# Kernel optimization log

Hardware: AMD Instinct MI355X
Metric: run time of the kernel (lower is better)

The kernel has to match this reference:

```python
import jax, jax.numpy as jnp
import numpy as np

TEMPERATURE = 0.5
NUM_NEG_CANDIDATES = 8
HARD_NEG_K = 3


def setup_inputs() -> dict:
    key = jax.random.key(0)
    k1, k2 = jax.random.split(key)
    features = jax.random.normal(k1, (8192, 512), dtype=jnp.float32)
    labels = jax.random.randint(k2, (8192,), 0, 64, dtype=jnp.int64)
    return {"features": features, "labels": labels}


def reference(features, labels):
    B = features.shape[0]
    labels = labels.reshape(-1)
    # L2-normalize rows (torch F.normalize, eps=1e-12)
    f = features / jnp.maximum(jnp.linalg.norm(features, axis=1, keepdims=True), 1e-12)

    same = labels[:, None] == labels[None, :]          # [B, B]
    eye = jnp.eye(B, dtype=bool)
    neg_inf = jnp.float32(-jnp.inf)

    # Deterministic replacement for torch's randint/randperm sampling:
    # Gumbel-max = uniform sampling of one positive; Gumbel-top-m = sampling
    # m negatives without replacement.
    kp, kn = jax.random.split(jax.random.key(42))
    g_pos = jax.random.gumbel(kp, (B, B), dtype=jnp.float32)
    g_neg = jax.random.gumbel(kn, (B, B), dtype=jnp.float32)

    pos_mask = same & ~eye
    pos_j = jnp.argmax(jnp.where(pos_mask, g_pos, neg_inf), axis=1)   # [B]

    _, neg_idx = jax.lax.top_k(jnp.where(~same, g_neg, neg_inf), NUM_NEG_CANDIDATES)  # [B, m]

    cand = f[neg_idx]                                  # [B, m, D]
    neg_sims = jnp.einsum('bd,bmd->bm', f, cand)       # [B, m]
    hard_sims, _ = jax.lax.top_k(neg_sims, HARD_NEG_K)  # [B, k] hardest negatives

    pos_logit = jnp.sum(f * f[pos_j], axis=1) / TEMPERATURE          # [B]
    logits = jnp.concatenate([pos_logit[:, None], hard_sims / TEMPERATURE], axis=1)  # [B, 1+k]
    # cross-entropy with target index 0
    loss = jax.nn.logsumexp(logits, axis=1) - logits[:, 0]
    return jnp.mean(loss)
```

## Files before the change

### kernel.cpp

```cpp
#include <hip/hip_runtime.h>
#include <hip/hip_bf16.h>
#include <stdint.h>

#define BB 8192
#define DD 512
#define NNEG 8
#define CAP 256

#define VTHI 4273471488u

__host__ __device__ __forceinline__ uint32_t rotl32(uint32_t x, int r) {
#if defined(__HIP_DEVICE_COMPILE__)
  return __builtin_amdgcn_alignbit(x, x, 32 - r);
#else
  return (x << r) | (x >> (32 - r));
#endif
}

#define TF_RND(x0, x1, R) { x0 += x1; x1 = rotl32(x1, R); x1 ^= x0; }

__host__ __device__ __forceinline__ void threefry2x32(uint32_t k0, uint32_t k1,
                                                      uint32_t x0, uint32_t x1,
                                                      uint32_t& o0, uint32_t& o1) {
  uint32_t ks2 = k0 ^ k1 ^ 0x1BD11BDAu;
  x0 += k0; x1 += k1;
  TF_RND(x0, x1, 13) TF_RND(x0, x1, 15) TF_RND(x0, x1, 26) TF_RND(x0, x1, 6)
  x0 += k1; x1 += ks2 + 1u;
  TF_RND(x0, x1, 17) TF_RND(x0, x1, 29) TF_RND(x0, x1, 16) TF_RND(x0, x1, 24)
  x0 += ks2; x1 += k0 + 2u;
  TF_RND(x0, x1, 13) TF_RND(x0, x1, 15) TF_RND(x0, x1, 26) TF_RND(x0, x1, 6)
  x0 += k0; x1 += k1 + 3u;
  TF_RND(x0, x1, 17) TF_RND(x0, x1, 29) TF_RND(x0, x1, 16) TF_RND(x0, x1, 24)
  x0 += k1; x1 += ks2 + 4u;
  TF_RND(x0, x1, 13) TF_RND(x0, x1, 15) TF_RND(x0, x1, 26) TF_RND(x0, x1, 6)
  x0 += ks2; x1 += k0 + 5u;
  o0 = x0; o1 = x1;
}

__device__ __forceinline__ void tf_uniform(uint32_t k0, uint32_t k1, uint32_t x1pk,
                                           uint32_t& o0, uint32_t& o1) {
  uint32_t ks2 = k0 ^ k1 ^ 0x1BD11BDAu;
  uint32_t x0 = k0;
  uint32_t x1 = x1pk;
  TF_RND(x0, x1, 13) TF_RND(x0, x1, 15) TF_RND(x0, x1, 26) TF_RND(x0, x1, 6)
  x0 += k1; x1 += ks2 + 1u;
  TF_RND(x0, x1, 17) TF_RND(x0, x1, 29) TF_RND(x0, x1, 16) TF_RND(x0, x1, 24)
  x0 += ks2; x1 += k0 + 2u;
  TF_RND(x0, x1, 13) TF_RND(x0, x1, 15) TF_RND(x0, x1, 26) TF_RND(x0, x1, 6)
  x0 += k0; x1 += k1 + 3u;
  TF_RND(x0, x1, 17) TF_RND(x0, x1, 29) TF_RND(x0, x1, 16) TF_RND(x0, x1, 24)
  x0 += k1; x1 += ks2 + 4u;
  TF_RND(x0, x1, 13) TF_RND(x0, x1, 15) TF_RND(x0, x1, 26) TF_RND(x0, x1, 6)
  x0 += ks2; x1 += k0 + 5u;
  o0 = x0; o1 = x1;
}

__device__ __forceinline__ unsigned long long u64max(unsigned long long a, unsigned long long b) {
  return a > b ? a : b;
}
#define CE_DESC(m, x, y) { if (m[x] < m[y]) { unsigned long long _t = m[x]; m[x] = m[y]; m[y] = _t; } }
#define TOP8_INSERT(top, key) \
  if ((key) > top[7]) { \
    top[7] = (key); \
    _Pragma("unroll") \
    for (int s = 7; s > 0; --s) { \
      if (top[s] > top[s - 1]) { \
        unsigned long long _tt = top[s - 1]; top[s - 1] = top[s]; top[s] = _tt; \
      } \
    } \
  }

__device__ __forceinline__ void wave_merge_top8(unsigned long long top[8]) {
  #pragma unroll
  for (int d = 1; d < 64; d <<= 1) {
    unsigned long long o[8];
    #pragma unroll
    for (int r = 0; r < 8; ++r) o[r] = __shfl_xor(top[r], d, 64);
    unsigned long long m[8];
    #pragma unroll
    for (int r = 0; r < 8; ++r) m[r] = u64max(top[r], o[7 - r]);
    CE_DESC(m, 0, 4) CE_DESC(m, 1, 5) CE_DESC(m, 2, 6) CE_DESC(m, 3, 7)
    CE_DESC(m, 0, 2) CE_DESC(m, 1, 3) CE_DESC(m, 4, 6) CE_DESC(m, 5, 7)
    CE_DESC(m, 0, 1) CE_DESC(m, 2, 3) CE_DESC(m, 4, 5) CE_DESC(m, 6, 7)
    #pragma unroll
    for (int r = 0; r < 8; ++r) top[r] = m[r];
  }
}

__global__ __launch_bounds__(256) void prep_kernel(const float* __restrict__ feat,
                                                   const int* __restrict__ labels,
                                                   float* __restrict__ inv_norm,
                                                   uint16_t* __restrict__ lists,
                                                   int* __restrict__ offs) {
  if (blockIdx.x == 0) {
    __shared__ uint32_t hist[64];
    __shared__ uint32_t base[64];
    int t = threadIdx.x;
    if (t < 64) hist[t] = 0u;
    __syncthreads();
    for (int e = t; e < BB; e += 256) atomicAdd(&hist[labels[e] & 63], 1u);
    __syncthreads();
    if (t == 0) {
      uint32_t s = 0;
      for (int l = 0; l < 64; ++l) { base[l] = s; offs[l] = (int)s; s += hist[l]; }
      offs[64] = (int)s;
    }
    __syncthreads();
    for (int e = t; e < BB; e += 256) {
      uint32_t p = atomicAdd(&base[labels[e] & 63], 1u);
      lists[p] = (uint16_t)e;
    }
  } else {
    int wave = threadIdx.x >> 6, lane = threadIdx.x & 63;
    int row = (blockIdx.x - 1) * 4 + wave;
    const float4* fr = (const float4*)(feat + (size_t)row * DD);
    float4 a = fr[lane], b = fr[lane + 64];
    float s = a.x * a.x + a.y * a.y + a.z * a.z + a.w * a.w
            + b.x * b.x + b.y * b.y + b.z * b.z + b.w * b.w;
    #pragma unroll
    for (int d = 1; d < 64; d <<= 1) s += __shfl_xor(s, d, 64);
    if (lane == 0) inv_norm[row] = 1.0f / fmaxf(sqrtf(s), 1e-12f);
  }
}

__global__ __launch_bounds__(256) void select_kernel(const float* __restrict__ feat,
                                                     const int* __restrict__ labels,
                                                     const float* __restrict__ inv_norm,
                                                     const uint16_t* __restrict__ lists,
                                                     const int* __restrict__ offs,
                                                     uint32_t kp0, uint32_t kp1,
                                                     uint32_t kn0, uint32_t kn1,
                                                     float* __restrict__ out) {
  __shared__ uint2 buf[4][CAP];
  __shared__ uint32_t cnt[4];
  __shared__ float part[4];
  int wave = threadIdx.x >> 6, lane = threadIdx.x & 63;
  int i = blockIdx.x * 4 + wave;
  if (threadIdx.x < 4) cnt[threadIdx.x] = 0u;
  __syncthreads();

  int li = labels[i];
  uint32_t rowbase = (uint32_t)i * (uint32_t)BB;

  uint32_t cb = rowbase + kn1 + (uint32_t)lane;
  #pragma unroll 8
  for (int it = 0; it < BB / 64; ++it) {
    uint32_t o0, o1;
    tf_uniform(kn0, kn1, cb + (uint32_t)(it * 64), o0, o1);
    uint32_t bits = o0 ^ o1;
    if (bits >= VTHI) {
      uint32_t p = atomicAdd(&cnt[wave], 1u);
      if (p < CAP) { uint2 e; e.x = bits; e.y = (uint32_t)(it * 64 + lane); buf[wave][p] = e; }
    }
  }

  unsigned long long best = 0ull;
  int beg = offs[li], end = offs[li + 1];
  for (int t = beg + lane; t < end; t += 64) {
    int j = lists[t];
    if (j != i) {
      uint32_t o0, o1;
      tf_uniform(kp0, kp1, rowbase + kp1 + (uint32_t)j, o0, o1);
      unsigned long long key =
          (((unsigned long long)((o0 ^ o1) >> 9) << 13) | (unsigned)(8191 - j)) + 1ull;
      best = u64max(best, key);
    }
  }
  #pragma unroll
  for (int d = 1; d < 64; d <<= 1) best = u64max(best, __shfl_xor(best, d, 64));

  uint32_t count = cnt[wave];
  unsigned long long top[8] = {0ull,0ull,0ull,0ull,0ull,0ull,0ull,0ull};
  if (count <= CAP) {
    for (int t = lane; t < (int)count; t += 64) {
      uint2 e = buf[wave][t];
      uint32_t j = e.y;
      if (labels[j] != li) {
        unsigned long long key =
            (((unsigned long long)(e.x >> 9) << 13) | (unsigned)(8191u - j)) + 1ull;
        TOP8_INSERT(top, key)
      }
    }
  } else {
    for (int j = lane; j < BB; j += 64) {
      if (labels[j] != li) {
        uint32_t o0, o1;
        tf_uniform(kn0, kn1, rowbase + kn1 + (uint32_t)j, o0, o1);
        unsigned long long key =
            (((unsigned long long)((o0 ^ o1) >> 9) << 13) | (unsigned)(8191 - j)) + 1ull;
        TOP8_INSERT(top, key)
      }
    }
  }
  wave_merge_top8(top);

  uint32_t hi = VTHI;
  while (top[7] == 0ull && hi != 0u) {
    unsigned long long W = 0x100000000ull - (unsigned long long)hi;
    uint32_t newhi = (W * 8ull >= 0x100000000ull) ? 0u
                     : (uint32_t)(0x100000000ull - W * 8ull);
    for (int j = lane; j < BB; j += 64) {
      if (labels[j] != li) {
        uint32_t o0, o1;
        tf_uniform(kn0, kn1, rowbase + kn1 + (uint32_t)j, o0, o1);
        uint32_t bits = o0 ^ o1;
        if (bits >= newhi && bits < hi) {
          unsigned long long key =
              (((unsigned long long)(bits >> 9) << 13) | (unsigned)(8191 - j)) + 1ull;
          TOP8_INSERT(top, key)
        }
      }
    }
    wave_merge_top8(top);
    hi = newhi;
  }

  int cand[9];
  cand[0] = best ? (8191 - (int)((best - 1ull) & 0x1FFFull)) : 0;
  #pragma unroll
  for (int r = 0; r < NNEG; ++r)
    cand[r + 1] = top[r] ? (8191 - (int)((top[r] - 1ull) & 0x1FFFull)) : r;

  const float4* fi = (const float4*)(feat + (size_t)i * DD);
  float4 a0 = fi[lane], a1 = fi[lane + 64];
  float dots[9];
  #pragma unroll
  for (int c = 0; c < 9; ++c) {
    const float4* fc = (const float4*)(feat + (size_t)cand[c] * DD);
    float4 c0 = fc[lane], c1 = fc[lane + 64];
    float s;
    s = a0.x * c0.x;
    s = fmaf(a0.y, c0.y, s); s = fmaf(a0.z, c0.z, s); s = fmaf(a0.w, c0.w, s);
    s = fmaf(a1.x, c1.x, s); s = fmaf(a1.y, c1.y, s);
    s = fmaf(a1.z, c1.z, s); s = fmaf(a1.w, c1.w, s);
    dots[c] = s;
  }
  #pragma unroll
  for (int c = 0; c < 9; ++c) {
    #pragma unroll
    for (int d = 1; d < 64; d <<= 1) dots[c] += __shfl_xor(dots[c], d, 64);
  }

  if (lane == 0) {
    float inv_i = inv_norm[i];
    float pos = dots[0] * inv_i * inv_norm[cand[0]] * 2.0f;
    float t1 = -1e30f, t2 = -1e30f, t3 = -1e30f;
    #pragma unroll
    for (int m = 0; m < NNEG; ++m) {
      float v = dots[m + 1] * inv_i * inv_norm[cand[m + 1]] * 2.0f;
      if (v > t1)      { t3 = t2; t2 = t1; t1 = v; }
      else if (v > t2) { t3 = t2; t2 = v; }
      else if (v > t3) { t3 = v; }
    }
    float mx = fmaxf(fmaxf(pos, t1), fmaxf(t2, t3));
    float lse = mx + logf(__expf(pos - mx) + __expf(t1 - mx) + __expf(t2 - mx) + __expf(t3 - mx));
    part[wave] = (lse - pos) * (1.0f / (float)BB);
  }
  __syncthreads();
  if (threadIdx.x == 0) atomicAdd(out, part[0] + part[1] + part[2] + part[3]);
}

extern "C" void kernel_launch(void* const* d_in, const int* in_sizes, int n_in,
                              void* d_out, int out_size, void* d_ws, size_t ws_size,
                              hipStream_t stream) {
  const float* features = (const float*)d_in[0];
  const int* labels = (const int*)d_in[1];
  float* out = (float*)d_out;

  float* inv_norm = (float*)d_ws;
  uint16_t* lists = (uint16_t*)((char*)d_ws + BB * sizeof(float));
  int* offs = (int*)((char*)d_ws + BB * sizeof(float) + BB * sizeof(uint16_t));

  uint32_t kp0, kp1, kn0, kn1;
  threefry2x32(0u, 42u, 0u, 0u, kp0, kp1);
  threefry2x32(0u, 42u, 0u, 1u, kn0, kn1);

  hipMemsetAsync(d_out, 0, sizeof(float), stream);
  prep_kernel<<<BB / 4 + 1, 256, 0, stream>>>(features, labels, inv_norm, lists, offs);
  select_kernel<<<BB / 4, 256, 0, stream>>>(features, labels, inv_norm, lists, offs,
                                            kp0, kp1, kn0, kn1, out);
}
```

Before: 254.4 us.

## Split select kernel into scan and loss kernels with ballot compaction and 4-way RNG ILP

Splits the fused select kernel into an RNG scan kernel that writes positive and negative indices to workspace, and a separate loss kernel that gathers candidate rows and computes the loss. The scan generates four independent threefry streams per iteration to expose instruction-level parallelism. It also replaces the per-candidate LDS atomic counter with wave ballot plus mbcnt compaction. The loss kernel issues all nine candidate row loads before computing dot products. The split lets each kernel use fewer registers and overlap memory better, at the cost of an extra launch and index traffic through global memory.

```diff
diff --git a/kernel.cpp b/kernel.cpp
--- a/kernel.cpp
+++ b/kernel.cpp
@@ -40,8 +40,7 @@
 __device__ __forceinline__ void tf_uniform(uint32_t k0, uint32_t k1, uint32_t x1pk,
                                            uint32_t& o0, uint32_t& o1) {
   uint32_t ks2 = k0 ^ k1 ^ 0x1BD11BDAu;
-  uint32_t x0 = k0;
-  uint32_t x1 = x1pk;
+  uint32_t x0 = k0, x1 = x1pk;
   TF_RND(x0, x1, 13) TF_RND(x0, x1, 15) TF_RND(x0, x1, 26) TF_RND(x0, x1, 6)
   x0 += k1; x1 += ks2 + 1u;
   TF_RND(x0, x1, 17) TF_RND(x0, x1, 29) TF_RND(x0, x1, 16) TF_RND(x0, x1, 24)
@@ -53,6 +52,30 @@
   TF_RND(x0, x1, 13) TF_RND(x0, x1, 15) TF_RND(x0, x1, 26) TF_RND(x0, x1, 6)
   x0 += ks2; x1 += k0 + 5u;
   o0 = x0; o1 = x1;
+}
+
+#define RND4(R) { TF_RND(x0a, x1a, R) TF_RND(x0b, x1b, R) TF_RND(x0c, x1c, R) TF_RND(x0d, x1d, R) }
+#define INJ4(A, B) { uint32_t _b = (B); \
+  x0a += (A); x1a += _b; x0b += (A); x1b += _b; x0c += (A); x1c += _b; x0d += (A); x1d += _b; }
+
+__device__ __forceinline__ void tf_uniform4(uint32_t k0, uint32_t k1, uint32_t ctr,
+                                            uint32_t bits[4]) {
+  uint32_t ks2 = k0 ^ k1 ^ 0x1BD11BDAu;
+  uint32_t x0a = k0, x1a = ctr;
+  uint32_t x0b = k0, x1b = ctr + 64u;
+  uint32_t x0c = k0, x1c = ctr + 128u;
+  uint32_t x0d = k0, x1d = ctr + 192u;
+  RND4(13) RND4(15) RND4(26) RND4(6)
+  INJ4(k1, ks2 + 1u)
+  RND4(17) RND4(29) RND4(16) RND4(24)
+  INJ4(ks2, k0 + 2u)
+  RND4(13) RND4(15) RND4(26) RND4(6)
+  INJ4(k0, k1 + 3u)
+  RND4(17) RND4(29) RND4(16) RND4(24)
+  INJ4(k1, ks2 + 4u)
+  RND4(13) RND4(15) RND4(26) RND4(6)
+  INJ4(ks2, k0 + 5u)
+  bits[0] = x0a ^ x1a; bits[1] = x0b ^ x1b; bits[2] = x0c ^ x1c; bits[3] = x0d ^ x1d;
 }
 
 __device__ __forceinline__ unsigned long long u64max(unsigned long long a, unsigned long long b) {
@@ -123,34 +146,40 @@
   }
 }
 
-__global__ __launch_bounds__(256) void select_kernel(const float* __restrict__ feat,
-                                                     const int* __restrict__ labels,
-                                                     const float* __restrict__ inv_norm,
-                                                     const uint16_t* __restrict__ lists,
-                                                     const int* __restrict__ offs,
-                                                     uint32_t kp0, uint32_t kp1,
-                                                     uint32_t kn0, uint32_t kn1,
-                                                     float* __restrict__ out) {
+__global__ __launch_bounds__(256) void scan_kernel(const int* __restrict__ labels,
+                                                   const uint16_t* __restrict__ lists,
+                                                   const int* __restrict__ offs,
+                                                   uint32_t kp0, uint32_t kp1,
+                                                   uint32_t kn0, uint32_t kn1,
+                                                   int* __restrict__ pos_j,
+                                                   int* __restrict__ neg_idx) {
   __shared__ uint2 buf[4][CAP];
-  __shared__ uint32_t cnt[4];
-  __shared__ float part[4];
   int wave = threadIdx.x >> 6, lane = threadIdx.x & 63;
   int i = blockIdx.x * 4 + wave;
-  if (threadIdx.x < 4) cnt[threadIdx.x] = 0u;
-  __syncthreads();
-
   int li = labels[i];
   uint32_t rowbase = (uint32_t)i * (uint32_t)BB;
+  uint32_t count = 0;
 
   uint32_t cb = rowbase + kn1 + (uint32_t)lane;
-  #pragma unroll 8
-  for (int it = 0; it < BB / 64; ++it) {
-    uint32_t o0, o1;
-    tf_uniform(kn0, kn1, cb + (uint32_t)(it * 64), o0, o1);
-    uint32_t bits = o0 ^ o1;
-    if (bits >= VTHI) {
-      uint32_t p = atomicAdd(&cnt[wave], 1u);
-      if (p < CAP) { uint2 e; e.x = bits; e.y = (uint32_t)(it * 64 + lane); buf[wave][p] = e; }
+  for (int it = 0; it < BB / 256; ++it) {
+    uint32_t bits[4];
+    tf_uniform4(kn0, kn1, cb + (uint32_t)(it * 256), bits);
+    #pragma unroll
+    for (int c = 0; c < 4; ++c) {
+      bool cand = bits[c] >= VTHI;
+      unsigned long long m = __ballot(cand);
+      if (m) {
+        if (cand) {
+          int ofs = __builtin_amdgcn_mbcnt_hi((uint32_t)(m >> 32),
+                     __builtin_amdgcn_mbcnt_lo((uint32_t)m, 0));
+          uint32_t p = count + (uint32_t)ofs;
+          if (p < CAP) {
+            uint2 e; e.x = bits[c]; e.y = (uint32_t)(it * 256 + c * 64 + lane);
+            buf[wave][p] = e;
+          }
+        }
+        count += (uint32_t)__popcll(m);
+      }
     }
   }
 
@@ -169,7 +198,6 @@
   #pragma unroll
   for (int d = 1; d < 64; d <<= 1) best = u64max(best, __shfl_xor(best, d, 64));
 
-  uint32_t count = cnt[wave];
   unsigned long long top[8] = {0ull,0ull,0ull,0ull,0ull,0ull,0ull,0ull};
   if (count <= CAP) {
     for (int t = lane; t < (int)count; t += 64) {
@@ -215,24 +243,45 @@
     hi = newhi;
   }
 
-  int cand[9];
-  cand[0] = best ? (8191 - (int)((best - 1ull) & 0x1FFFull)) : 0;
-  #pragma unroll
-  for (int r = 0; r < NNEG; ++r)
-    cand[r + 1] = top[r] ? (8191 - (int)((top[r] - 1ull) & 0x1FFFull)) : r;
-
+  if (lane == 0) {
+    pos_j[i] = best ? (8191 - (int)((best - 1ull) & 0x1FFFull)) : 0;
+    #pragma unroll
+    for (int r = 0; r < NNEG; ++r)
+      neg_idx[i * 8 + r] = top[r] ? (8191 - (int)((top[r] - 1ull) & 0x1FFFull)) : r;
+  }
+}
+
+__global__ __launch_bounds__(256) void loss_kernel(const float* __restrict__ feat,
+                                                   const float* __restrict__ inv_norm,
+                                                   const int* __restrict__ pos_j,
+                                                   const int* __restrict__ neg_idx,
+                                                   float* __restrict__ out) {
+  __shared__ float part[4];
+  int wave = threadIdx.x >> 6, lane = threadIdx.x & 63;
+  int i = blockIdx.x * 4 + wave;
   const float4* fi = (const float4*)(feat + (size_t)i * DD);
   float4 a0 = fi[lane], a1 = fi[lane + 64];
-  float dots[9];
+
+  int cand[9];
+  cand[0] = pos_j[i];
+  #pragma unroll
+  for (int m = 0; m < NNEG; ++m) cand[m + 1] = neg_idx[i * 8 + m];
+
+  float4 c0[9], c1[9];
   #pragma unroll
   for (int c = 0; c < 9; ++c) {
     const float4* fc = (const float4*)(feat + (size_t)cand[c] * DD);
-    float4 c0 = fc[lane], c1 = fc[lane + 64];
+    c0[c] = fc[lane];
+    c1[c] = fc[lane + 64];
+  }
+  float dots[9];
+  #pragma unroll
+  for (int c = 0; c < 9; ++c) {
     float s;
-    s = a0.x * c0.x;
-    s = fmaf(a0.y, c0.y, s); s = fmaf(a0.z, c0.z, s); s = fmaf(a0.w, c0.w, s);
-    s = fmaf(a1.x, c1.x, s); s = fmaf(a1.y, c1.y, s);
-    s = fmaf(a1.z, c1.z, s); s = fmaf(a1.w, c1.w, s);
+    s = a0.x * c0[c].x;
+    s = fmaf(a0.y, c0[c].y, s); s = fmaf(a0.z, c0[c].z, s); s = fmaf(a0.w, c0[c].w, s);
+    s = fmaf(a1.x, c1[c].x, s); s = fmaf(a1.y, c1[c].y, s);
+    s = fmaf(a1.z, c1[c].z, s); s = fmaf(a1.w, c1[c].w, s);
     dots[c] = s;
   }
   #pragma unroll
@@ -267,9 +316,12 @@
   const int* labels = (const int*)d_in[1];
   float* out = (float*)d_out;
 
-  float* inv_norm = (float*)d_ws;
-  uint16_t* lists = (uint16_t*)((char*)d_ws + BB * sizeof(float));
-  int* offs = (int*)((char*)d_ws + BB * sizeof(float) + BB * sizeof(uint16_t));
+  char* w = (char*)d_ws;
+  float* inv_norm = (float*)w;                    w += BB * sizeof(float);
+  uint16_t* lists = (uint16_t*)w;                 w += BB * sizeof(uint16_t);
+  int* offs = (int*)w;                            w += 65 * sizeof(int) + 28;
+  int* pos_j = (int*)w;                           w += BB * sizeof(int);
+  int* neg_idx = (int*)w;
 
   uint32_t kp0, kp1, kn0, kn1;
   threefry2x32(0u, 42u, 0u, 0u, kp0, kp1);
@@ -277,6 +329,7 @@
 
   hipMemsetAsync(d_out, 0, sizeof(float), stream);
   prep_kernel<<<BB / 4 + 1, 256, 0, stream>>>(features, labels, inv_norm, lists, offs);
-  select_kernel<<<BB / 4, 256, 0, stream>>>(features, labels, inv_norm, lists, offs,
-                                            kp0, kp1, kn0, kn1, out);
-}
+  scan_kernel<<<BB / 4, 256, 0, stream>>>(labels, lists, offs, kp0, kp1, kn0, kn1,
+                                          pos_j, neg_idx);
+  loss_kernel<<<BB / 4, 256, 0, stream>>>(features, inv_norm, pos_j, neg_idx, out);
+}
```

After: 292.8 us. 1.15x slower.
